# Performance work log

Measured on AMD Instinct MI355X. Metric: run time of the kernel, lower is better.

## Reference

```python
import jax, jax.numpy as jnp
import numpy as np

NUM_CAPSULES = 16
IN_DIM = 512
OUT_DIM = 32
ROUTING_ITERS = 3
EPS = 1e-08


def setup_inputs() -> dict:
    key = jax.random.key(0)
    kx, kw = jax.random.split(key)
    x = jax.random.normal(kx, (32768, IN_DIM), dtype=jnp.float32)
    W = jax.random.normal(kw, (IN_DIM, NUM_CAPSULES * OUT_DIM), dtype=jnp.float32)
    return {"x": x, "W": W}


def squash(s):
    # s: [batch, out_dim]
    norm = jnp.sum(s * s, axis=-1, keepdims=True)
    scale = norm / (1.0 + norm)
    return scale * s / (jnp.sqrt(norm) + EPS)


def reference(x, W):
    batch = x.shape[0]
    # u: [batch, num_capsules, out_dim]
    u = jnp.matmul(x, W).reshape(batch, NUM_CAPSULES, OUT_DIM)
    b = jnp.zeros((batch, NUM_CAPSULES), dtype=x.dtype)
    v = None
    for _ in range(ROUTING_ITERS):
        c = jax.nn.softmax(b, axis=1)[..., None]       # [batch, caps, 1]
        s = jnp.sum(c * u, axis=1)                      # [batch, out_dim]
        v = squash(s)                                   # [batch, out_dim]
        b = b + jnp.sum(u * v[:, None, :], axis=-1)     # [batch, caps]
    return v
```

## Files before the change

### kernel.cpp

```cpp
#include <hip/hip_runtime.h>
#include <math.h>


#define BATCH   32768
#define KDIM    512
#define NDIM    512
#define OUT_DIM 32
#define EPS_F   1e-8f
#define NKT     32
#define KPS     8
#define NSB     4

typedef _Float16 half8  __attribute__((ext_vector_type(8)));
typedef _Float16 half4t __attribute__((ext_vector_type(4)));
typedef float   floatx4 __attribute__((ext_vector_type(4)));
typedef float  floatx16 __attribute__((ext_vector_type(16)));

template <int CTRL>
__device__ __forceinline__ float dpp_mov(float x) {
    return __int_as_float(__builtin_amdgcn_mov_dpp(__float_as_int(x), CTRL, 0xF, 0xF, true));
}
template <int XMASK>
__device__ __forceinline__ float swz_xor(float x) {
    return __int_as_float(__builtin_amdgcn_ds_swizzle(__float_as_int(x), (XMASK << 10) | 31));
}
#define ROR4  0x124
#define ROR8  0x128
#define QXOR1 0xB1
#define QXOR2 0x4E

__device__ __forceinline__ float cap_sum(float x) {
    x += dpp_mov<ROR4>(x);
    x += dpp_mov<ROR8>(x);
    x += swz_xor<16>(x);
    x += __shfl_xor(x, 32);
    return x;
}
__device__ __forceinline__ float cap_max(float x) {
    x = fmaxf(x, dpp_mov<ROR4>(x));
    x = fmaxf(x, dpp_mov<ROR8>(x));
    x = fmaxf(x, swz_xor<16>(x));
    x = fmaxf(x, __shfl_xor(x, 32));
    return x;
}
__device__ __forceinline__ float dg_sum(float x) {
    x += dpp_mov<QXOR1>(x);
    x += dpp_mov<QXOR2>(x);
    return x;
}

__global__ void prep_w(const float* __restrict__ W, _Float16* __restrict__ Wh,
                       _Float16* __restrict__ Wl) {
    __shared__ float tile[32][33];
    const int tx = threadIdx.x, ty = threadIdx.y;
    const int n0 = blockIdx.x * 32, k0 = blockIdx.y * 32;
#pragma unroll
    for (int i = 0; i < 4; ++i)
        tile[ty + 8 * i][tx] = W[(size_t)(k0 + ty + 8 * i) * NDIM + n0 + tx];
    __syncthreads();
#pragma unroll
    for (int i = 0; i < 4; ++i) {
        const int k = k0 + tx, n = n0 + ty + 8 * i;
        const float v = tile[tx][ty + 8 * i];
        const _Float16 h = (_Float16)v;
        const _Float16 l = (_Float16)(v - (float)h);
        const size_t off = (size_t)(k >> 4) * (NDIM * 16) + (size_t)n * 16 + (k & 15);
        Wh[off] = h;
        Wl[off] = l;
    }
}

__global__ __launch_bounds__(256, 2)
void capsule_mfma(const float* __restrict__ x, const _Float16* __restrict__ Wh,
                  const _Float16* __restrict__ Wl, float* __restrict__ out) {
    __shared__ __align__(16) char smem[66560];
    float (*u_lds)[520] = (float (*)[520])smem;

    const int tid  = threadIdx.x;
    const int w    = tid >> 6;
    const int lane = tid & 63;
    const int ln = lane & 31, q = lane >> 5;
    const int rowBlk = blockIdx.x * 64;
    const int C0 = w * 128;

    floatx16 acc[2][4];
#pragma unroll
    for (int mf = 0; mf < 2; ++mf)
#pragma unroll
        for (int nt = 0; nt < 4; ++nt)
#pragma unroll
            for (int i = 0; i < 16; ++i) acc[mf][nt][i] = 0.f;

    const int srow0 = tid >> 5;
    const int sf    = tid & 31;
    const int skt   = sf >> 2;
    const int skq   = sf & 3;
    const float* aga = x + (size_t)(rowBlk + srow0) * KDIM + skt * 16 + skq * 4;
    const int ssw = (srow0 >> 1) & 3;
    const int woffh = skt * 4096 + srow0 * 64 + (((skq >> 1) ^ ssw) * 16) + (skq & 1) * 8;

    const int hoff0 = ln * 64 + ((q ^ ((ln >> 1) & 3)) * 16);

    const int boff = (C0 + ln) * 16 + q * 8;

    {
        floatx4 s0[8];
#pragma unroll
        for (int i = 0; i < 8; ++i)
            s0[i] = *(const floatx4*)(aga + (size_t)(8 * i) * KDIM);
#pragma unroll
        for (int i = 0; i < 8; ++i) {
            half4t h4, l4;
#pragma unroll
            for (int j = 0; j < 4; ++j) {
                h4[j] = (_Float16)s0[i][j];
                l4[j] = (_Float16)(s0[i][j] - (float)h4[j]);
            }
            *(half4t*)(smem + woffh + i * 512)        = h4;
            *(half4t*)(smem + (woffh ^ 32) + i * 512) = l4;
        }
    }
    half8 bh[2], bl[2];
    bh[0] = *(const half8*)(Wh + boff);
    bl[0] = *(const half8*)(Wl + boff);

#define COMPUTE_KK(kk)                                                          \
    {                                                                           \
        const int kt = s * KPS + (kk);                                          \
        const char* ab = smem + abuf + (kk) * 4096;                             \
        const half8 ah0 = *(const half8*)(ab + hoff0);                          \
        const half8 al0 = *(const half8*)(ab + (hoff0 ^ 32));                   \
        const half8 ah1 = *(const half8*)(ab + hoff0 + 2048);                   \
        const half8 al1 = *(const half8*)(ab + ((hoff0 + 2048) ^ 32));          \
        _Pragma("unroll")                                                       \
        for (int nt = 0; nt < 4; ++nt) {                                        \
            const int cu = nt & 1, nx = cu ^ 1;                                 \
            const int kn = (nt < 3) ? kt : ((kt + 1 < NKT) ? kt + 1 : kt);      \
            const int nn = (nt < 3) ? nt + 1 : 0;                               \
            bh[nx] = *(const half8*)(Wh + (size_t)kn * 8192 + nn * 512 + boff); \
            bl[nx] = *(const half8*)(Wl + (size_t)kn * 8192 + nn * 512 + boff); \
            acc[0][nt] = __builtin_amdgcn_mfma_f32_32x32x16_f16(ah0, bh[cu], acc[0][nt], 0, 0, 0); \
            acc[0][nt] = __builtin_amdgcn_mfma_f32_32x32x16_f16(al0, bh[cu], acc[0][nt], 0, 0, 0); \
            acc[0][nt] = __builtin_amdgcn_mfma_f32_32x32x16_f16(ah0, bl[cu], acc[0][nt], 0, 0, 0); \
            acc[1][nt] = __builtin_amdgcn_mfma_f32_32x32x16_f16(ah1, bh[cu], acc[1][nt], 0, 0, 0); \
            acc[1][nt] = __builtin_amdgcn_mfma_f32_32x32x16_f16(al1, bh[cu], acc[1][nt], 0, 0, 0); \
            acc[1][nt] = __builtin_amdgcn_mfma_f32_32x32x16_f16(ah1, bl[cu], acc[1][nt], 0, 0, 0); \
        }                                                                       \
    }

#define STAGE_HALF(h0)                                                          \
    {                                                                           \
        half4t h4, l4;                                                          \
        _Pragma("unroll")                                                       \
        for (int i = 0; i < 4; ++i) {                                           \
            _Pragma("unroll")                                                   \
            for (int j = 0; j < 4; ++j) {                                       \
                h4[j] = (_Float16)sv[i][j];                                     \
                l4[j] = (_Float16)(sv[i][j] - (float)h4[j]);                    \
            }                                                                   \
            *(half4t*)(smem + nbuf + woffh + ((h0) + i) * 512)        = h4;     \
            *(half4t*)(smem + nbuf + ((woffh ^ 32)) + ((h0) + i) * 512) = l4;   \
        }                                                                       \
    }

#pragma unroll 1
    for (int s = 0; s < NSB; ++s) {
        __syncthreads();
        const int abuf = (s & 1) * 32768;
        const int nbuf = abuf ^ 32768;
        floatx4 sv[4];
        if (s + 1 < NSB) {
#pragma unroll
            for (int i = 0; i < 4; ++i)
                sv[i] = *(const floatx4*)(aga + (size_t)(s + 1) * 128 + (size_t)(8 * i) * KDIM);
        }
        COMPUTE_KK(0)
        COMPUTE_KK(1)
        if (s + 1 < NSB) STAGE_HALF(0)
        if (s + 1 < NSB) {
#pragma unroll
            for (int i = 0; i < 4; ++i)
                sv[i] = *(const floatx4*)(aga + (size_t)(s + 1) * 128 + (size_t)(8 * (i + 4)) * KDIM);
        }
        COMPUTE_KK(2)
        COMPUTE_KK(3)
        COMPUTE_KK(4)
        COMPUTE_KK(5)
        if (s + 1 < NSB) STAGE_HALF(4)
        COMPUTE_KK(6)
        COMPUTE_KK(7)
    }

    const int dgrp = lane & 3;
#pragma unroll
    for (int p = 0; p < 2; ++p) {
        __syncthreads();
        {
            const int mf = p;
#pragma unroll
            for (int nt = 0; nt < 4; ++nt)
#pragma unroll
                for (int reg = 0; reg < 16; ++reg)
                    u_lds[(reg & 3) + 8 * (reg >> 2) + 4 * q][C0 + nt * 32 + ln] = acc[mf][nt][reg];
        }
        __syncthreads();
#pragma unroll 1
        for (int ri = 0; ri < 8; ++ri) {
            const int rl = w * 8 + ri;
            const floatx4 ua = *(const floatx4*)&u_lds[rl][lane * 8];
            const floatx4 ub = *(const floatx4*)&u_lds[rl][lane * 8 + 4];
            const float u8[8] = {ua[0], ua[1], ua[2], ua[3],
                                 ub[0], ub[1], ub[2], ub[3]};
            float b_own = 0.f;
            float v[8];
#pragma unroll
            for (int it = 0; it < 3; ++it) {
                float c_own;
                if (it == 0) {
                    c_own = 1.0f / 16.0f;
                } else {
                    const float m = cap_max(b_own);
                    const float e = __expf(b_own - m);
                    const float ssum = cap_sum(e);
                    c_own = e / ssum;
                }
                float s8[8];
#pragma unroll
                for (int j = 0; j < 8; ++j) s8[j] = c_own * u8[j];
#pragma unroll
                for (int j = 0; j < 8; ++j) s8[j] += dpp_mov<ROR4>(s8[j]);
#pragma unroll
                for (int j = 0; j < 8; ++j) s8[j] += dpp_mov<ROR8>(s8[j]);
#pragma unroll
                for (int j = 0; j < 8; ++j) s8[j] += swz_xor<16>(s8[j]);
#pragma unroll
                for (int j = 0; j < 8; ++j) s8[j] += __shfl_xor(s8[j], 32);
                float nrm = 0.f;
#pragma unroll
                for (int j = 0; j < 8; ++j) nrm = fmaf(s8[j], s8[j], nrm);
                nrm = dg_sum(nrm);
                const float scale = nrm / ((1.f + nrm) * (sqrtf(nrm) + EPS_F));
#pragma unroll
                for (int j = 0; j < 8; ++j) v[j] = scale * s8[j];
                if (it < 2) {
                    float dot = 0.f;
#pragma unroll
                    for (int j = 0; j < 8; ++j) dot = fmaf(u8[j], v[j], dot);
                    dot = dg_sum(dot);
                    b_own += dot;
                }
            }
            if (lane < 4) {
                float4* o = (float4*)(out + (size_t)(rowBlk + p * 32 + rl) * OUT_DIM
                                      + dgrp * 8);
                o[0] = make_float4(v[0], v[1], v[2], v[3]);
                o[1] = make_float4(v[4], v[5], v[6], v[7]);
            }
        }
    }
}

extern "C" void kernel_launch(void* const* d_in, const int* in_sizes, int n_in,
                              void* d_out, int out_size, void* d_ws, size_t ws_size,
                              hipStream_t stream) {
    const float* x = (const float*)d_in[0];
    const float* W = (const float*)d_in[1];
    float* out = (float*)d_out;
    _Float16* Wh = (_Float16*)d_ws;
    _Float16* Wl = Wh + (size_t)NDIM * KDIM;

    prep_w<<<dim3(16, 16), dim3(32, 8), 0, stream>>>(W, Wh, Wl);
    capsule_mfma<<<dim3(BATCH / 64), dim3(256), 0, stream>>>(x, Wh, Wl, out);
}
```

Before: 158.5 us.

## Interleave hi/lo weight halves and prefetch a full k-tile of B fragments

Packs the fp16 high and low parts of W into one interleaved buffer, so each lane's hi and lo fragments sit 32 bytes apart. The main loop now keeps all four n-tile B fragments in registers and prefetches the next k-tile's fragments after issuing the MFMAs, instead of a two-deep rotating prefetch. The intent is to give global loads more time to land before use and to improve locality. x loads and output stores switch to nontemporal hints so streaming data does not pollute the cache. The deeper B prefetch doubles B fragment registers, which may raise pressure under the 2-blocks-per-SM launch bound.

```diff
diff --git a/kernel.cpp b/kernel.cpp
--- a/kernel.cpp
+++ b/kernel.cpp
@@ -49,8 +49,7 @@
     return x;
 }
 
-__global__ void prep_w(const float* __restrict__ W, _Float16* __restrict__ Wh,
-                       _Float16* __restrict__ Wl) {
+__global__ void prep_w(const float* __restrict__ W, _Float16* __restrict__ Whl) {
     __shared__ float tile[32][33];
     const int tx = threadIdx.x, ty = threadIdx.y;
     const int n0 = blockIdx.x * 32, k0 = blockIdx.y * 32;
@@ -64,15 +63,15 @@
         const float v = tile[tx][ty + 8 * i];
         const _Float16 h = (_Float16)v;
         const _Float16 l = (_Float16)(v - (float)h);
-        const size_t off = (size_t)(k >> 4) * (NDIM * 16) + (size_t)n * 16 + (k & 15);
-        Wh[off] = h;
-        Wl[off] = l;
+        const size_t off = (size_t)(k >> 4) * (NDIM * 32) + (size_t)n * 32 + (k & 15);
+        Whl[off]      = h;
+        Whl[off + 16] = l;
     }
 }
 
 __global__ __launch_bounds__(256, 2)
-void capsule_mfma(const float* __restrict__ x, const _Float16* __restrict__ Wh,
-                  const _Float16* __restrict__ Wl, float* __restrict__ out) {
+void capsule_mfma(const float* __restrict__ x, const _Float16* __restrict__ Whl,
+                  float* __restrict__ out) {
     __shared__ __align__(16) char smem[66560];
     float (*u_lds)[520] = (float (*)[520])smem;
 
@@ -101,13 +100,20 @@
 
     const int hoff0 = ln * 64 + ((q ^ ((ln >> 1) & 3)) * 16);
 
-    const int boff = (C0 + ln) * 16 + q * 8;
-
+    const int lane_off = (C0 + ln) * 32 + q * 8;
+
+    half8 bh[4], bl[4];
+#pragma unroll
+    for (int nt = 0; nt < 4; ++nt) {
+        const _Float16* bp = Whl + nt * 1024 + lane_off;
+        bh[nt] = *(const half8*)bp;
+        bl[nt] = *(const half8*)(bp + 16);
+    }
     {
         floatx4 s0[8];
 #pragma unroll
         for (int i = 0; i < 8; ++i)
-            s0[i] = *(const floatx4*)(aga + (size_t)(8 * i) * KDIM);
+            s0[i] = __builtin_nontemporal_load((const floatx4*)(aga + (size_t)(8 * i) * KDIM));
 #pragma unroll
         for (int i = 0; i < 8; ++i) {
             half4t h4, l4;
@@ -120,9 +126,6 @@
             *(half4t*)(smem + (woffh ^ 32) + i * 512) = l4;
         }
     }
-    half8 bh[2], bl[2];
-    bh[0] = *(const half8*)(Wh + boff);
-    bl[0] = *(const half8*)(Wl + boff);
 
 #define COMPUTE_KK(kk)                                                          \
     {                                                                           \
@@ -132,19 +135,18 @@
         const half8 al0 = *(const half8*)(ab + (hoff0 ^ 32));                   \
         const half8 ah1 = *(const half8*)(ab + hoff0 + 2048);                   \
         const half8 al1 = *(const half8*)(ab + ((hoff0 + 2048) ^ 32));          \
+        const int ktn = (kt + 1 < NKT) ? kt + 1 : kt;                           \
+        const _Float16* bkt = Whl + (size_t)ktn * 16384 + lane_off;             \
         _Pragma("unroll")                                                       \
         for (int nt = 0; nt < 4; ++nt) {                                        \
-            const int cu = nt & 1, nx = cu ^ 1;                                 \
-            const int kn = (nt < 3) ? kt : ((kt + 1 < NKT) ? kt + 1 : kt);      \
-            const int nn = (nt < 3) ? nt + 1 : 0;                               \
-            bh[nx] = *(const half8*)(Wh + (size_t)kn * 8192 + nn * 512 + boff); \
-            bl[nx] = *(const half8*)(Wl + (size_t)kn * 8192 + nn * 512 + boff); \
-            acc[0][nt] = __builtin_amdgcn_mfma_f32_32x32x16_f16(ah0, bh[cu], acc[0][nt], 0, 0, 0); \
-            acc[0][nt] = __builtin_amdgcn_mfma_f32_32x32x16_f16(al0, bh[cu], acc[0][nt], 0, 0, 0); \
-            acc[0][nt] = __builtin_amdgcn_mfma_f32_32x32x16_f16(ah0, bl[cu], acc[0][nt], 0, 0, 0); \
-            acc[1][nt] = __builtin_amdgcn_mfma_f32_32x32x16_f16(ah1, bh[cu], acc[1][nt], 0, 0, 0); \
-            acc[1][nt] = __builtin_amdgcn_mfma_f32_32x32x16_f16(al1, bh[cu], acc[1][nt], 0, 0, 0); \
-            acc[1][nt] = __builtin_amdgcn_mfma_f32_32x32x16_f16(ah1, bl[cu], acc[1][nt], 0, 0, 0); \
+            acc[0][nt] = __builtin_amdgcn_mfma_f32_32x32x16_f16(ah0, bh[nt], acc[0][nt], 0, 0, 0); \
+            acc[0][nt] = __builtin_amdgcn_mfma_f32_32x32x16_f16(al0, bh[nt], acc[0][nt], 0, 0, 0); \
+            acc[1][nt] = __builtin_amdgcn_mfma_f32_32x32x16_f16(ah1, bh[nt], acc[1][nt], 0, 0, 0); \
+            acc[1][nt] = __builtin_amdgcn_mfma_f32_32x32x16_f16(al1, bh[nt], acc[1][nt], 0, 0, 0); \
+            acc[0][nt] = __builtin_amdgcn_mfma_f32_32x32x16_f16(ah0, bl[nt], acc[0][nt], 0, 0, 0); \
+            acc[1][nt] = __builtin_amdgcn_mfma_f32_32x32x16_f16(ah1, bl[nt], acc[1][nt], 0, 0, 0); \
+            bh[nt] = *(const half8*)(bkt + nt * 1024);                          \
+            bl[nt] = *(const half8*)(bkt + nt * 1024 + 16);                     \
         }                                                                       \
     }
 
@@ -172,7 +174,8 @@
         if (s + 1 < NSB) {
 #pragma unroll
             for (int i = 0; i < 4; ++i)
-                sv[i] = *(const floatx4*)(aga + (size_t)(s + 1) * 128 + (size_t)(8 * i) * KDIM);
+                sv[i] = __builtin_nontemporal_load(
+                    (const floatx4*)(aga + (size_t)(s + 1) * 128 + (size_t)(8 * i) * KDIM));
         }
         COMPUTE_KK(0)
         COMPUTE_KK(1)
@@ -180,7 +183,8 @@
         if (s + 1 < NSB) {
 #pragma unroll
             for (int i = 0; i < 4; ++i)
-                sv[i] = *(const floatx4*)(aga + (size_t)(s + 1) * 128 + (size_t)(8 * (i + 4)) * KDIM);
+                sv[i] = __builtin_nontemporal_load(
+                    (const floatx4*)(aga + (size_t)(s + 1) * 128 + (size_t)(8 * (i + 4)) * KDIM));
         }
         COMPUTE_KK(2)
         COMPUTE_KK(3)
@@ -251,10 +255,11 @@
                 }
             }
             if (lane < 4) {
-                float4* o = (float4*)(out + (size_t)(rowBlk + p * 32 + rl) * OUT_DIM
-                                      + dgrp * 8);
-                o[0] = make_float4(v[0], v[1], v[2], v[3]);
-                o[1] = make_float4(v[4], v[5], v[6], v[7]);
+                float* o = out + (size_t)(rowBlk + p * 32 + rl) * OUT_DIM + dgrp * 8;
+                floatx4 o0 = {v[0], v[1], v[2], v[3]};
+                floatx4 o1 = {v[4], v[5], v[6], v[7]};
+                __builtin_nontemporal_store(o0, (floatx4*)o);
+                __builtin_nontemporal_store(o1, (floatx4*)(o + 4));
             }
         }
     }
@@ -266,9 +271,8 @@
     const float* x = (const float*)d_in[0];
     const float* W = (const float*)d_in[1];
     float* out = (float*)d_out;
-    _Float16* Wh = (_Float16*)d_ws;
-    _Float16* Wl = Wh + (size_t)NDIM * KDIM;
-
-    prep_w<<<dim3(16, 16), dim3(32, 8), 0, stream>>>(W, Wh, Wl);
-    capsule_mfma<<<dim3(BATCH / 64), dim3(256), 0, stream>>>(x, Wh, Wl, out);
-}
+    _Float16* Whl = (_Float16*)d_ws;
+
+    prep_w<<<dim3(16, 16), dim3(32, 8), 0, stream>>>(W, Whl);
+    capsule_mfma<<<dim3(BATCH / 64), dim3(256), 0, stream>>>(x, Whl, out);
+}
```

After: 167.0 us. 5.3% more time.
